# Kernel optimization log

Hardware: AMD Instinct MI355X
Metric: run time of the kernel (lower is better)

The kernel has to match this reference:

```python
import jax, jax.numpy as jnp
import numpy as np

N = 50000      # nodes
E = 600000     # edges
F_IN = 128     # num_features
H = 128        # conv_dim
C = 10         # num_classes


def setup_inputs() -> dict:
    key = jax.random.key(0)
    ks = jax.random.split(key, 16)
    s = 0.05
    return {
        "x": jax.random.normal(ks[0], (N, F_IN), jnp.float32),
        "edge_index": jax.random.randint(ks[1], (2, E), 0, N, dtype=jnp.int32),
        "W1": jax.random.normal(ks[2], (F_IN, H), jnp.float32) * s,
        "b1": jnp.zeros((H,), jnp.float32),
        "W2": jax.random.normal(ks[3], (H, H), jnp.float32) * s,
        "b2": jnp.zeros((H,), jnp.float32),
        "W3": jax.random.normal(ks[4], (H, H), jnp.float32) * s,
        "b3": jnp.zeros((H,), jnp.float32),
        "fw1": jax.random.normal(ks[5], (3 * H, 128), jnp.float32) * s,
        "fb1": jnp.zeros((128,), jnp.float32),
        "fw2": jax.random.normal(ks[6], (128, 64), jnp.float32) * s,
        "fb2": jnp.zeros((64,), jnp.float32),
        "fw3": jax.random.normal(ks[7], (64, C), jnp.float32) * s,
        "fb3": jnp.zeros((C,), jnp.float32),
    }


def reference(x, edge_index, W1, b1, W2, b2, W3, b3, fw1, fb1, fw2, fb2, fw3, fb3):
    n = x.shape[0]
    # GCN normalization with self-loops (improved=False): A_hat = D^-1/2 (A+I) D^-1/2
    loop = jnp.arange(n, dtype=edge_index.dtype)
    src = jnp.concatenate([edge_index[0], loop])   # [E+N]
    tgt = jnp.concatenate([edge_index[1], loop])   # [E+N]
    deg = jax.ops.segment_sum(jnp.ones_like(src, dtype=x.dtype), tgt, num_segments=n)
    dis = jnp.where(deg > 0, jax.lax.rsqrt(jnp.maximum(deg, 1e-12)), 0.0)
    norm = dis[src] * dis[tgt]                     # [E+N]

    def gcn(h, W, b):
        hw = h @ W                                 # [N,H] linear transform first
        msg = norm[:, None] * hw[src]              # gather + edge scale
        return jax.ops.segment_sum(msg, tgt, num_segments=n) + b  # scatter-add

    x1 = jax.nn.relu(gcn(x, W1, b1))
    x2 = jax.nn.relu(gcn(x1, W2, b2))
    x3 = jax.nn.relu(gcn(x2, W3, b3))
    h = jnp.sum(jnp.concatenate([x1, x2, x3], axis=1), axis=0)  # [3H] sum pool
    h = jax.nn.relu(h @ fw1 + fb1)
    h = jax.nn.relu(h @ fw2 + fb2)
    return h @ fw3 + fb3
```

## Files before the change

### kernel.cpp

```cpp
#include <hip/hip_runtime.h>

#define FDIM 128

typedef __attribute__((ext_vector_type(8))) short bf16x8;
typedef __attribute__((ext_vector_type(4))) float f32x4;
typedef __attribute__((ext_vector_type(2))) float f32x2;


__device__ __forceinline__ unsigned int cvt_bf16(float f) {
    unsigned int u = __float_as_uint(f);
    return (u + 0x7fffu + ((u >> 16) & 1u)) >> 16;
}



__global__ void hist_kernel(const int* __restrict__ tgt, int* __restrict__ count, int ne) {
    int e = blockIdx.x * blockDim.x + threadIdx.x;
    if (e < ne) atomicAdd(&count[tgt[e]], 1);
}

__global__ __launch_bounds__(256) void scan1_kernel(const int* __restrict__ count,
                                                    float* __restrict__ dis,
                                                    int* __restrict__ tpre,
                                                    int* __restrict__ bsum, int n) {
    __shared__ int sm[256];
    int tid = threadIdx.x, blk = blockIdx.x;
    int base = blk * 2048 + tid * 8;
    int s = 0;
    #pragma unroll
    for (int q = 0; q < 8; q++) {
        int i = base + q;
        if (i < n) {
            int c = count[i];
            s += c;
            dis[i] = rsqrtf((float)(c + 1));
        }
    }
    sm[tid] = s;
    __syncthreads();
    for (int off = 1; off < 256; off <<= 1) {
        int v = sm[tid];
        int u = (tid >= off) ? sm[tid - off] : 0;
        __syncthreads();
        sm[tid] = v + u;
        __syncthreads();
    }
    tpre[blk * 256 + tid] = (tid == 0) ? 0 : sm[tid - 1];
    if (tid == 255) bsum[blk] = sm[255];
}

__global__ __launch_bounds__(1024) void scan2_kernel(const int* __restrict__ bsum,
                                                     int* __restrict__ bpre,
                                                     int* __restrict__ rowptr,
                                                     float* __restrict__ pool,
                                                     int n, int nb) {
    __shared__ int sm[1024];
    int tid = threadIdx.x;
    if (tid < 384) pool[tid] = 0.f;
    sm[tid] = (tid < nb) ? bsum[tid] : 0;
    __syncthreads();
    for (int off = 1; off < 1024; off <<= 1) {
        int v = sm[tid];
        int u = (tid >= off) ? sm[tid - off] : 0;
        __syncthreads();
        sm[tid] = v + u;
        __syncthreads();
    }
    if (tid < nb) bpre[tid] = (tid == 0) ? 0 : sm[tid - 1];
    if (tid == nb - 1) rowptr[n] = sm[tid];
}

__global__ __launch_bounds__(256) void scan3_kernel(const int* __restrict__ count,
                                                    const int* __restrict__ tpre,
                                                    const int* __restrict__ bpre,
                                                    int* __restrict__ rowptr,
                                                    int* __restrict__ cursor, int n) {
    int tid = threadIdx.x, blk = blockIdx.x;
    int run = bpre[blk] + tpre[blk * 256 + tid];
    int base = blk * 2048 + tid * 8;
    #pragma unroll
    for (int q = 0; q < 8; q++) {
        int i = base + q;
        if (i < n) {
            rowptr[i] = run;
            cursor[i] = run;
            run += count[i];
        }
    }
}

__global__ void fill_kernel(const int* __restrict__ src, const int* __restrict__ tgt,
                            int* __restrict__ cursor, int* __restrict__ csrs, int ne) {
    int e = blockIdx.x * blockDim.x + threadIdx.x;
    if (e < ne) {
        int t = tgt[e];
        int s = src[e];
        int slot = atomicAdd(&cursor[t], 1);
        csrs[slot] = s;
    }
}


__global__ void prep_kernel(const float* __restrict__ W1, const float* __restrict__ W2,
                            const float* __restrict__ W3,
                            unsigned* __restrict__ B1, unsigned* __restrict__ B2,
                            unsigned* __restrict__ B3,
                            unsigned short* __restrict__ g8,
                            int* __restrict__ count, int n) {
    int i = blockIdx.x * blockDim.x + threadIdx.x;
    if (i < 3 * 8192) {
        int w = i >> 13;
        int jj = i & 8191;
        const float* W = (w == 0) ? W1 : (w == 1) ? W2 : W3;
        unsigned* B    = (w == 0) ? B1 : (w == 1) ? B2 : B3;
        int nn = jj >> 6, u = jj & 63;
        float lo = W[(size_t)u * 128 + nn];
        float hi = W[(size_t)(u + 64) * 128 + nn];
        B[jj] = cvt_bf16(lo) | (cvt_bf16(hi) << 16);
    } else if (i < 3 * 8192 + 64) {
        g8[(size_t)n * 64 + (i - 3 * 8192)] = 0;
    } else {
        int k = i - (3 * 8192 + 64);
        if (k < n) count[k] = 0;
    }
}


__global__ __launch_bounds__(256) void gemm_kernel(const unsigned* __restrict__ A16,
                                                   const float* __restrict__ A32,
                                                   const unsigned* __restrict__ Bt16,
                                                   const float* __restrict__ dis,
                                                   unsigned short* __restrict__ g8, int n) {
    int tid  = threadIdx.x;
    int wave = tid >> 6, lane = tid & 63;
    int quad = lane >> 4, r16 = lane & 15;
    int m0 = (blockIdx.x * 4 + wave) * 16;
    if (m0 >= n) return;

    f32x4 acc[8] = {};

    #pragma unroll
    for (int ks = 0; ks < 4; ks++) {
        int m = m0 + r16;
        if (m >= n) m = n - 1;
        int u0 = ks * 16 + quad * 4;
        bf16x8 af;
        if (A32) {
            float4 lo = *(const float4*)(A32 + (size_t)m * 128 + u0);
            float4 hi = *(const float4*)(A32 + (size_t)m * 128 + u0 + 64);
            uint4 p;
            p.x = cvt_bf16(lo.x) | (cvt_bf16(hi.x) << 16);
            p.y = cvt_bf16(lo.y) | (cvt_bf16(hi.y) << 16);
            p.z = cvt_bf16(lo.z) | (cvt_bf16(hi.z) << 16);
            p.w = cvt_bf16(lo.w) | (cvt_bf16(hi.w) << 16);
            af = *(bf16x8*)&p;
        } else {
            uint4 av = *(const uint4*)(A16 + (size_t)m * 64 + u0);
            af = *(bf16x8*)&av;
        }
        #pragma unroll
        for (int t = 0; t < 8; t++) {
            int ncol = t * 16 + r16;
            uint4 bv = *(const uint4*)(Bt16 + (size_t)ncol * 64 + u0);
            bf16x8 bf = *(bf16x8*)&bv;
            acc[t] = __builtin_amdgcn_mfma_f32_16x16x32_bf16(af, bf, acc[t], 0, 0, 0);
        }
    }

    #pragma unroll
    for (int r = 0; r < 4; r++) {
        int row = m0 + quad * 4 + r;
        if (row < n) {
            float dr = dis[row];
            #pragma unroll
            for (int t = 0; t < 4; t++) {
                int p = __builtin_amdgcn_cvt_pk_fp8_f32(dr * acc[t][r], dr * acc[t + 4][r], 0, false);
                g8[(size_t)row * 64 + t * 16 + r16] = (unsigned short)(p & 0xffff);
            }
        }
    }
}


#define AGG_ACC(v)                                                     \
    { f32x2 p;                                                         \
      p = __builtin_amdgcn_cvt_pk_f32_fp8((int)v.x, 0); f0[0]+=p.x; f1[0]+=p.y; \
      p = __builtin_amdgcn_cvt_pk_f32_fp8((int)v.x, 1); f0[1]+=p.x; f1[1]+=p.y; \
      p = __builtin_amdgcn_cvt_pk_f32_fp8((int)v.y, 0); f0[2]+=p.x; f1[2]+=p.y; \
      p = __builtin_amdgcn_cvt_pk_f32_fp8((int)v.y, 1); f0[3]+=p.x; f1[3]+=p.y; \
      p = __builtin_amdgcn_cvt_pk_f32_fp8((int)v.z, 0); f0[4]+=p.x; f1[4]+=p.y; \
      p = __builtin_amdgcn_cvt_pk_f32_fp8((int)v.z, 1); f0[5]+=p.x; f1[5]+=p.y; \
      p = __builtin_amdgcn_cvt_pk_f32_fp8((int)v.w, 0); f0[6]+=p.x; f1[6]+=p.y; \
      p = __builtin_amdgcn_cvt_pk_f32_fp8((int)v.w, 1); f0[7]+=p.x; f1[7]+=p.y; }

#define ISSUE1(buf, ereg, EBASE, mlim)                                 \
    { int e = (EBASE) + j;                                             \
      int s = __shfl(ereg, e);                                         \
      if (e >= (mlim)) s = n;                                          \
      buf = *(const uint4*)(g8 + (size_t)(unsigned)s * 64u + c * 8); }

#define ROUND4(ereg, Q0, mlim)                                         \
    { uint4 u0, u1, u2, u3;                                            \
      ISSUE1(u0, ereg, (Q0) + 0, mlim)                                 \
      if ((mlim) > (Q0) + 8)  ISSUE1(u1, ereg, (Q0) + 8,  mlim)        \
      if ((mlim) > (Q0) + 16) ISSUE1(u2, ereg, (Q0) + 16, mlim)        \
      if ((mlim) > (Q0) + 24) ISSUE1(u3, ereg, (Q0) + 24, mlim)        \
      AGG_ACC(u0)                                                      \
      if ((mlim) > (Q0) + 8)  AGG_ACC(u1)                              \
      if ((mlim) > (Q0) + 16) AGG_ACC(u2)                              \
      if ((mlim) > (Q0) + 24) AGG_ACC(u3) }

__global__ __launch_bounds__(512) void agg_kernel(const unsigned short* __restrict__ g8,
                                                  const float* __restrict__ dis,
                                                  const int* __restrict__ rowptr,
                                                  const int* __restrict__ csrs,
                                                  const float* __restrict__ bias,
                                                  unsigned* __restrict__ out16,
                                                  float* __restrict__ pool,
                                                  int n, int nbase, int nend) {
    __shared__ float lpool[128];
    int tid = threadIdx.x;
    if (tid < 128) lpool[tid] = 0.f;
    __syncthreads();

    int wave = tid >> 6, lane = tid & 63;
    int j = lane >> 3;
    int c = lane & 7;
    int node0 = nbase + (blockIdx.x * 8 + wave) * 4;

    float b0[8], b1[8];
    *(float4*)&b0[0] = *(const float4*)(bias + c * 8);
    *(float4*)&b0[4] = *(const float4*)(bias + c * 8 + 4);
    *(float4*)&b1[0] = *(const float4*)(bias + 64 + c * 8);
    *(float4*)&b1[4] = *(const float4*)(bias + 64 + c * 8 + 4);

    int rpv = 0; float dv = 0.f;
    if (lane <= 4) rpv = rowptr[min(node0 + lane, nend)];
    if (lane < 4)  dv  = dis[min(node0 + lane, n - 1)];

    int er[4];
    #pragma unroll
    for (int i = 0; i < 4; i++) {
        int beg = __shfl(rpv, i);
        er[i] = csrs[beg + lane];
    }

    uint4 c0, c1, c2, c3, sB;
    {
        int deg = __shfl(rpv, 1) - __shfl(rpv, 0);
        int mlim = min(deg, 64);
        int ereg = er[0];
        ISSUE1(c0, ereg, 0, mlim)
        if (deg > 8)  ISSUE1(c1, ereg, 8,  mlim)
        if (deg > 16) ISSUE1(c2, ereg, 16, mlim)
        if (deg > 24) ISSUE1(c3, ereg, 24, mlim)
        int s = (node0 < nend && j == 0) ? node0 : n;
        sB = *(const uint4*)(g8 + (size_t)(unsigned)s * 64u + c * 8);
    }

    float pp0[8] = {}, pp1[8] = {};

    #pragma unroll
    for (int i = 0; i < 4; i++) {
        int node = node0 + i;
        bool ok = node < nend;
        int beg = __shfl(rpv, i);
        int end = __shfl(rpv, i + 1);
        int deg = end - beg;
        float di = __shfl(dv, i);

        float f0[8] = {}, f1[8] = {};
        AGG_ACC(c0)
        if (deg > 8)  AGG_ACC(c1)
        if (deg > 16) AGG_ACC(c2)
        if (deg > 24) AGG_ACC(c3)
        if (deg > 32) {
            int mlim = min(deg, 64);
            ROUND4(er[i], 32, mlim)
            for (int b2 = 64; b2 < deg; b2 += 64) {
                int ereg2 = csrs[beg + b2 + lane];
                int ml2 = min(deg - b2, 64);
                ROUND4(ereg2, 0, ml2)
                if (ml2 > 32) ROUND4(ereg2, 32, ml2)
            }
        }

        uint4 n0v, n1v, n2v, n3v, nS;
        if (i < 3) {
            int nd = __shfl(rpv, i + 2) - end;
            int nml = min(nd, 64);
            int ner = er[i + 1];
            ISSUE1(n0v, ner, 0, nml)
            if (nd > 8)  ISSUE1(n1v, ner, 8,  nml)
            if (nd > 16) ISSUE1(n2v, ner, 16, nml)
            if (nd > 24) ISSUE1(n3v, ner, 24, nml)
            int s = (node + 1 < nend && j == 0) ? (node + 1) : n;
            nS = *(const uint4*)(g8 + (size_t)(unsigned)s * 64u + c * 8);
        }

        #pragma unroll
        for (int k = 0; k < 8; k++) {
            f0[k] += __shfl_xor(f0[k], 8);  f1[k] += __shfl_xor(f1[k], 8);
            f0[k] += __shfl_xor(f0[k], 16); f1[k] += __shfl_xor(f1[k], 16);
            f0[k] += __shfl_xor(f0[k], 32); f1[k] += __shfl_xor(f1[k], 32);
        }
        if (j == 0) AGG_ACC(sB)

        if (ok) {
            float r0[8], r1[8];
            #pragma unroll
            for (int k = 0; k < 8; k++) {
                r0[k] = fmaxf(di * f0[k] + b0[k], 0.f);
                r1[k] = fmaxf(di * f1[k] + b1[k], 0.f);
                pp0[k] += r0[k];
                pp1[k] += r1[k];
            }
            if (out16 && j == 0) {
                uint4 wa, wb;
                wa.x = cvt_bf16(r0[0]) | (cvt_bf16(r1[0]) << 16);
                wa.y = cvt_bf16(r0[1]) | (cvt_bf16(r1[1]) << 16);
                wa.z = cvt_bf16(r0[2]) | (cvt_bf16(r1[2]) << 16);
                wa.w = cvt_bf16(r0[3]) | (cvt_bf16(r1[3]) << 16);
                wb.x = cvt_bf16(r0[4]) | (cvt_bf16(r1[4]) << 16);
                wb.y = cvt_bf16(r0[5]) | (cvt_bf16(r1[5]) << 16);
                wb.z = cvt_bf16(r0[6]) | (cvt_bf16(r1[6]) << 16);
                wb.w = cvt_bf16(r0[7]) | (cvt_bf16(r1[7]) << 16);
                *(uint4*)(out16 + (size_t)node * 64 + c * 8)     = wa;
                *(uint4*)(out16 + (size_t)node * 64 + c * 8 + 4) = wb;
            }
        }

        c0 = n0v; c1 = n1v; c2 = n2v; c3 = n3v; sB = nS;
    }

    if (j == 0) {
        #pragma unroll
        for (int k = 0; k < 8; k++) {
            atomicAdd(&lpool[c * 8 + k],      pp0[k]);
            atomicAdd(&lpool[64 + c * 8 + k], pp1[k]);
        }
    }
    __syncthreads();
    if (tid < 128) atomicAdd(&pool[tid], lpool[tid]);
}


__global__ __launch_bounds__(128) void mlp_kernel(const float* __restrict__ pool,
                                                  const float* __restrict__ fw1, const float* __restrict__ fb1,
                                                  const float* __restrict__ fw2, const float* __restrict__ fb2,
                                                  const float* __restrict__ fw3, const float* __restrict__ fb3,
                                                  float* __restrict__ out) {
    __shared__ float h0[384];
    __shared__ float h1[128];
    __shared__ float h2[64];
    int tid = threadIdx.x;
    for (int i = tid; i < 384; i += 128) h0[i] = pool[i];
    __syncthreads();
    {
        float s = fb1[tid];
        for (int k = 0; k < 384; k++) s += h0[k] * fw1[k * 128 + tid];
        h1[tid] = fmaxf(s, 0.f);
    }
    __syncthreads();
    if (tid < 64) {
        float s = fb2[tid];
        for (int k = 0; k < 128; k++) s += h1[k] * fw2[k * 64 + tid];
        h2[tid] = fmaxf(s, 0.f);
    }
    __syncthreads();
    if (tid < 10) {
        float s = fb3[tid];
        for (int k = 0; k < 64; k++) s += h2[k] * fw3[k * 10 + tid];
        out[tid] = s;
    }
}


extern "C" void kernel_launch(void* const* d_in, const int* in_sizes, int n_in,
                              void* d_out, int out_size, void* d_ws, size_t ws_size,
                              hipStream_t stream) {
    const float* x   = (const float*)d_in[0];
    const int*   ei  = (const int*)d_in[1];
    const float* W1  = (const float*)d_in[2];
    const float* b1  = (const float*)d_in[3];
    const float* W2  = (const float*)d_in[4];
    const float* b2  = (const float*)d_in[5];
    const float* W3  = (const float*)d_in[6];
    const float* b3  = (const float*)d_in[7];
    const float* fw1 = (const float*)d_in[8];
    const float* fb1 = (const float*)d_in[9];
    const float* fw2 = (const float*)d_in[10];
    const float* fb2 = (const float*)d_in[11];
    const float* fw3 = (const float*)d_in[12];
    const float* fb3 = (const float*)d_in[13];
    float* out = (float*)d_out;

    const int n  = in_sizes[0] / FDIM;
    const int ne = in_sizes[1] / 2;
    const int* src = ei;
    const int* tgt = ei + ne;

    char* ws = (char*)d_ws;
    size_t packBytes = (size_t)n * 64 * sizeof(unsigned);
    unsigned* A2   = (unsigned*)ws;  ws += packBytes;
    unsigned* A3   = (unsigned*)ws;  ws += packBytes;
    unsigned short* g8 = (unsigned short*)ws; ws += (((size_t)(n + 1) * 64 * 2 + 127) / 128) * 128;
    unsigned* B1t  = (unsigned*)ws;  ws += 128 * 64 * 4;
    unsigned* B2t  = (unsigned*)ws;  ws += 128 * 64 * 4;
    unsigned* B3t  = (unsigned*)ws;  ws += 128 * 64 * 4;
    float* dis  = (float*)ws;        ws += (size_t)n * 4;
    int* count  = (int*)ws;          ws += (size_t)n * 4;
    int* rowptr = (int*)ws;          ws += ((size_t)(n + 4) * 4 / 16) * 16;
    int* cursor = (int*)ws;          ws += (size_t)n * 4;
    int* csrs   = (int*)ws;          ws += (size_t)(ne + 64) * 4;
    float* pool = (float*)ws;        ws += 384 * 4;
    int nb = (n + 2047) / 2048;
    int* tpre = (int*)ws;            ws += (size_t)nb * 256 * 4;
    int* bsum = (int*)ws;            ws += ((size_t)(nb + 3) / 4) * 16;
    int* bpre = (int*)ws;            ws += ((size_t)(nb + 3) / 4) * 16;

    int prepTotal = 3 * 8192 + 64 + n;
    prep_kernel<<<(prepTotal + 255) / 256, 256, 0, stream>>>(W1, W2, W3, B1t, B2t, B3t, g8, count, n);

    hist_kernel<<<(ne + 255) / 256, 256, 0, stream>>>(tgt, count, ne);
    scan1_kernel<<<nb, 256, 0, stream>>>(count, dis, tpre, bsum, n);
    scan2_kernel<<<1, 1024, 0, stream>>>(bsum, bpre, rowptr, pool, n, nb);
    scan3_kernel<<<nb, 256, 0, stream>>>(count, tpre, bpre, rowptr, cursor, n);
    fill_kernel<<<(ne + 255) / 256, 256, 0, stream>>>(src, tgt, cursor, csrs, ne);

    int gemmGrid = (n + 63) / 64;
    int half = ((n / 2) + 31) & ~31;
    int ag1 = (half + 31) / 32;
    int ag2 = ((n - half) + 31) / 32;

    gemm_kernel<<<gemmGrid, 256, 0, stream>>>((const unsigned*)nullptr, x, B1t, dis, g8, n);
    agg_kernel<<<ag1, 512, 0, stream>>>(g8, dis, rowptr, csrs, b1, A2, pool + 0, n, 0, half);
    agg_kernel<<<ag2, 512, 0, stream>>>(g8, dis, rowptr, csrs, b1, A2, pool + 0, n, half, n);

    gemm_kernel<<<gemmGrid, 256, 0, stream>>>(A2, (const float*)nullptr, B2t, dis, g8, n);
    agg_kernel<<<ag1, 512, 0, stream>>>(g8, dis, rowptr, csrs, b2, A3, pool + 128, n, 0, half);
    agg_kernel<<<ag2, 512, 0, stream>>>(g8, dis, rowptr, csrs, b2, A3, pool + 128, n, half, n);

    gemm_kernel<<<gemmGrid, 256, 0, stream>>>(A3, (const float*)nullptr, B3t, dis, g8, n);
    agg_kernel<<<ag1, 512, 0, stream>>>(g8, dis, rowptr, csrs, b3, (unsigned*)nullptr, pool + 256, n, 0, half);
    agg_kernel<<<ag2, 512, 0, stream>>>(g8, dis, rowptr, csrs, b3, (unsigned*)nullptr, pool + 256, n, half, n);

    mlp_kernel<<<1, 128, 0, stream>>>(pool, fw1, fb1, fw2, fb2, fw3, fb3, out);
}
```

Baseline: 512.2 us.

## Fuse all GCN stages into one cooperative persistent megakernel with grid syncs

Replaces the chain of separate kernels (prep, histogram, three-stage scan, CSR fill, three gemm/aggregate pairs, MLP) with a single cooperative kernel. The stages are separated by grid.sync, and the gemm and aggregation phases become grid-stride loops over tiles. The scan is simplified to one element per thread plus a single-block scan of the per-block sums. The aim is to remove per-launch overhead and inter-kernel gaps. In exchange it pays for twelve grid-wide barriers, runs every phase with one fixed grid and block size, and occupancy may drop from the larger register footprint.

Result: slower. 970.9 us (+89.6%).

```diff
diff --git a/kernel.cpp b/kernel.cpp
--- a/kernel.cpp
+++ b/kernel.cpp
@@ -1,11 +1,13 @@
 #include <hip/hip_runtime.h>
+#include <hip/hip_cooperative_groups.h>
 
 #define FDIM 128
+
+namespace cg = cooperative_groups;
 
 typedef __attribute__((ext_vector_type(8))) short bf16x8;
 typedef __attribute__((ext_vector_type(4))) float f32x4;
 typedef __attribute__((ext_vector_type(2))) float f32x2;
-
 
 __device__ __forceinline__ unsigned int cvt_bf16(float f) {
     unsigned int u = __float_as_uint(f);
@@ -14,168 +16,56 @@
 
 
 
-__global__ void hist_kernel(const int* __restrict__ tgt, int* __restrict__ count, int ne) {
-    int e = blockIdx.x * blockDim.x + threadIdx.x;
-    if (e < ne) atomicAdd(&count[tgt[e]], 1);
-}
-
-__global__ __launch_bounds__(256) void scan1_kernel(const int* __restrict__ count,
-                                                    float* __restrict__ dis,
-                                                    int* __restrict__ tpre,
-                                                    int* __restrict__ bsum, int n) {
-    __shared__ int sm[256];
-    int tid = threadIdx.x, blk = blockIdx.x;
-    int base = blk * 2048 + tid * 8;
-    int s = 0;
-    #pragma unroll
-    for (int q = 0; q < 8; q++) {
-        int i = base + q;
-        if (i < n) {
-            int c = count[i];
-            s += c;
-            dis[i] = rsqrtf((float)(c + 1));
-        }
-    }
-    sm[tid] = s;
-    __syncthreads();
-    for (int off = 1; off < 256; off <<= 1) {
-        int v = sm[tid];
-        int u = (tid >= off) ? sm[tid - off] : 0;
-        __syncthreads();
-        sm[tid] = v + u;
-        __syncthreads();
-    }
-    tpre[blk * 256 + tid] = (tid == 0) ? 0 : sm[tid - 1];
-    if (tid == 255) bsum[blk] = sm[255];
-}
-
-__global__ __launch_bounds__(1024) void scan2_kernel(const int* __restrict__ bsum,
-                                                     int* __restrict__ bpre,
-                                                     int* __restrict__ rowptr,
-                                                     float* __restrict__ pool,
-                                                     int n, int nb) {
-    __shared__ int sm[1024];
+__device__ __forceinline__ void gemm_phase(const unsigned* __restrict__ A16,
+                                           const float* __restrict__ A32,
+                                           const unsigned* __restrict__ Bt16,
+                                           const float* __restrict__ dis,
+                                           unsigned short* __restrict__ g8, int n) {
     int tid = threadIdx.x;
-    if (tid < 384) pool[tid] = 0.f;
-    sm[tid] = (tid < nb) ? bsum[tid] : 0;
-    __syncthreads();
-    for (int off = 1; off < 1024; off <<= 1) {
-        int v = sm[tid];
-        int u = (tid >= off) ? sm[tid - off] : 0;
-        __syncthreads();
-        sm[tid] = v + u;
-        __syncthreads();
-    }
-    if (tid < nb) bpre[tid] = (tid == 0) ? 0 : sm[tid - 1];
-    if (tid == nb - 1) rowptr[n] = sm[tid];
-}
-
-__global__ __launch_bounds__(256) void scan3_kernel(const int* __restrict__ count,
-                                                    const int* __restrict__ tpre,
-                                                    const int* __restrict__ bpre,
-                                                    int* __restrict__ rowptr,
-                                                    int* __restrict__ cursor, int n) {
-    int tid = threadIdx.x, blk = blockIdx.x;
-    int run = bpre[blk] + tpre[blk * 256 + tid];
-    int base = blk * 2048 + tid * 8;
-    #pragma unroll
-    for (int q = 0; q < 8; q++) {
-        int i = base + q;
-        if (i < n) {
-            rowptr[i] = run;
-            cursor[i] = run;
-            run += count[i];
-        }
-    }
-}
-
-__global__ void fill_kernel(const int* __restrict__ src, const int* __restrict__ tgt,
-                            int* __restrict__ cursor, int* __restrict__ csrs, int ne) {
-    int e = blockIdx.x * blockDim.x + threadIdx.x;
-    if (e < ne) {
-        int t = tgt[e];
-        int s = src[e];
-        int slot = atomicAdd(&cursor[t], 1);
-        csrs[slot] = s;
-    }
-}
-
-
-__global__ void prep_kernel(const float* __restrict__ W1, const float* __restrict__ W2,
-                            const float* __restrict__ W3,
-                            unsigned* __restrict__ B1, unsigned* __restrict__ B2,
-                            unsigned* __restrict__ B3,
-                            unsigned short* __restrict__ g8,
-                            int* __restrict__ count, int n) {
-    int i = blockIdx.x * blockDim.x + threadIdx.x;
-    if (i < 3 * 8192) {
-        int w = i >> 13;
-        int jj = i & 8191;
-        const float* W = (w == 0) ? W1 : (w == 1) ? W2 : W3;
-        unsigned* B    = (w == 0) ? B1 : (w == 1) ? B2 : B3;
-        int nn = jj >> 6, u = jj & 63;
-        float lo = W[(size_t)u * 128 + nn];
-        float hi = W[(size_t)(u + 64) * 128 + nn];
-        B[jj] = cvt_bf16(lo) | (cvt_bf16(hi) << 16);
-    } else if (i < 3 * 8192 + 64) {
-        g8[(size_t)n * 64 + (i - 3 * 8192)] = 0;
-    } else {
-        int k = i - (3 * 8192 + 64);
-        if (k < n) count[k] = 0;
-    }
-}
-
-
-__global__ __launch_bounds__(256) void gemm_kernel(const unsigned* __restrict__ A16,
-                                                   const float* __restrict__ A32,
-                                                   const unsigned* __restrict__ Bt16,
-                                                   const float* __restrict__ dis,
-                                                   unsigned short* __restrict__ g8, int n) {
-    int tid  = threadIdx.x;
     int wave = tid >> 6, lane = tid & 63;
     int quad = lane >> 4, r16 = lane & 15;
-    int m0 = (blockIdx.x * 4 + wave) * 16;
-    if (m0 >= n) return;
-
-    f32x4 acc[8] = {};
-
-    #pragma unroll
-    for (int ks = 0; ks < 4; ks++) {
-        int m = m0 + r16;
-        if (m >= n) m = n - 1;
-        int u0 = ks * 16 + quad * 4;
-        bf16x8 af;
-        if (A32) {
-            float4 lo = *(const float4*)(A32 + (size_t)m * 128 + u0);
-            float4 hi = *(const float4*)(A32 + (size_t)m * 128 + u0 + 64);
-            uint4 p;
-            p.x = cvt_bf16(lo.x) | (cvt_bf16(hi.x) << 16);
-            p.y = cvt_bf16(lo.y) | (cvt_bf16(hi.y) << 16);
-            p.z = cvt_bf16(lo.z) | (cvt_bf16(hi.z) << 16);
-            p.w = cvt_bf16(lo.w) | (cvt_bf16(hi.w) << 16);
-            af = *(bf16x8*)&p;
-        } else {
-            uint4 av = *(const uint4*)(A16 + (size_t)m * 64 + u0);
-            af = *(bf16x8*)&av;
-        }
+    int nT = (n + 127) >> 7;
+    for (int T = blockIdx.x; T < nT; T += gridDim.x) {
+        int m0 = T * 128 + wave * 16;
+        if (m0 >= n) continue;
+        f32x4 acc[8] = {};
         #pragma unroll
-        for (int t = 0; t < 8; t++) {
-            int ncol = t * 16 + r16;
-            uint4 bv = *(const uint4*)(Bt16 + (size_t)ncol * 64 + u0);
-            bf16x8 bf = *(bf16x8*)&bv;
-            acc[t] = __builtin_amdgcn_mfma_f32_16x16x32_bf16(af, bf, acc[t], 0, 0, 0);
-        }
-    }
-
-    #pragma unroll
-    for (int r = 0; r < 4; r++) {
-        int row = m0 + quad * 4 + r;
-        if (row < n) {
-            float dr = dis[row];
+        for (int ks = 0; ks < 4; ks++) {
+            int m = m0 + r16;
+            if (m >= n) m = n - 1;
+            int u0 = ks * 16 + quad * 4;
+            bf16x8 af;
+            if (A32) {
+                float4 lo = *(const float4*)(A32 + (size_t)m * 128 + u0);
+                float4 hi = *(const float4*)(A32 + (size_t)m * 128 + u0 + 64);
+                uint4 p;
+                p.x = cvt_bf16(lo.x) | (cvt_bf16(hi.x) << 16);
+                p.y = cvt_bf16(lo.y) | (cvt_bf16(hi.y) << 16);
+                p.z = cvt_bf16(lo.z) | (cvt_bf16(hi.z) << 16);
+                p.w = cvt_bf16(lo.w) | (cvt_bf16(hi.w) << 16);
+                af = *(bf16x8*)&p;
+            } else {
+                uint4 av = *(const uint4*)(A16 + (size_t)m * 64 + u0);
+                af = *(bf16x8*)&av;
+            }
             #pragma unroll
-            for (int t = 0; t < 4; t++) {
-                int p = __builtin_amdgcn_cvt_pk_fp8_f32(dr * acc[t][r], dr * acc[t + 4][r], 0, false);
-                g8[(size_t)row * 64 + t * 16 + r16] = (unsigned short)(p & 0xffff);
+            for (int t = 0; t < 8; t++) {
+                int ncol = t * 16 + r16;
+                uint4 bv = *(const uint4*)(Bt16 + (size_t)ncol * 64 + u0);
+                bf16x8 bf = *(bf16x8*)&bv;
+                acc[t] = __builtin_amdgcn_mfma_f32_16x16x32_bf16(af, bf, acc[t], 0, 0, 0);
+            }
+        }
+        #pragma unroll
+        for (int r = 0; r < 4; r++) {
+            int row = m0 + quad * 4 + r;
+            if (row < n) {
+                float dr = dis[row];
+                #pragma unroll
+                for (int t = 0; t < 4; t++) {
+                    int p = __builtin_amdgcn_cvt_pk_fp8_f32(dr * acc[t][r], dr * acc[t + 4][r], 0, false);
+                    g8[(size_t)row * 64 + t * 16 + r16] = (unsigned short)(p & 0xffff);
+                }
             }
         }
     }
@@ -210,15 +100,14 @@
       if ((mlim) > (Q0) + 16) AGG_ACC(u2)                              \
       if ((mlim) > (Q0) + 24) AGG_ACC(u3) }
 
-__global__ __launch_bounds__(512) void agg_kernel(const unsigned short* __restrict__ g8,
-                                                  const float* __restrict__ dis,
-                                                  const int* __restrict__ rowptr,
-                                                  const int* __restrict__ csrs,
-                                                  const float* __restrict__ bias,
-                                                  unsigned* __restrict__ out16,
-                                                  float* __restrict__ pool,
-                                                  int n, int nbase, int nend) {
-    __shared__ float lpool[128];
+__device__ __forceinline__ void agg_phase(const unsigned short* __restrict__ g8,
+                                          const float* __restrict__ dis,
+                                          const int* __restrict__ rowptr,
+                                          const int* __restrict__ csrs,
+                                          const float* __restrict__ bias,
+                                          unsigned* __restrict__ out16,
+                                          float* __restrict__ poolseg,
+                                          float* lpool, int n) {
     int tid = threadIdx.x;
     if (tid < 128) lpool[tid] = 0.f;
     __syncthreads();
@@ -226,7 +115,6 @@
     int wave = tid >> 6, lane = tid & 63;
     int j = lane >> 3;
     int c = lane & 7;
-    int node0 = nbase + (blockIdx.x * 8 + wave) * 4;
 
     float b0[8], b1[8];
     *(float4*)&b0[0] = *(const float4*)(bias + c * 8);
@@ -234,103 +122,106 @@
     *(float4*)&b1[0] = *(const float4*)(bias + 64 + c * 8);
     *(float4*)&b1[4] = *(const float4*)(bias + 64 + c * 8 + 4);
 
-    int rpv = 0; float dv = 0.f;
-    if (lane <= 4) rpv = rowptr[min(node0 + lane, nend)];
-    if (lane < 4)  dv  = dis[min(node0 + lane, n - 1)];
-
-    int er[4];
-    #pragma unroll
-    for (int i = 0; i < 4; i++) {
-        int beg = __shfl(rpv, i);
-        er[i] = csrs[beg + lane];
-    }
-
-    uint4 c0, c1, c2, c3, sB;
-    {
-        int deg = __shfl(rpv, 1) - __shfl(rpv, 0);
-        int mlim = min(deg, 64);
-        int ereg = er[0];
-        ISSUE1(c0, ereg, 0, mlim)
-        if (deg > 8)  ISSUE1(c1, ereg, 8,  mlim)
-        if (deg > 16) ISSUE1(c2, ereg, 16, mlim)
-        if (deg > 24) ISSUE1(c3, ereg, 24, mlim)
-        int s = (node0 < nend && j == 0) ? node0 : n;
-        sB = *(const uint4*)(g8 + (size_t)(unsigned)s * 64u + c * 8);
-    }
-
     float pp0[8] = {}, pp1[8] = {};
-
-    #pragma unroll
-    for (int i = 0; i < 4; i++) {
-        int node = node0 + i;
-        bool ok = node < nend;
-        int beg = __shfl(rpv, i);
-        int end = __shfl(rpv, i + 1);
-        int deg = end - beg;
-        float di = __shfl(dv, i);
-
-        float f0[8] = {}, f1[8] = {};
-        AGG_ACC(c0)
-        if (deg > 8)  AGG_ACC(c1)
-        if (deg > 16) AGG_ACC(c2)
-        if (deg > 24) AGG_ACC(c3)
-        if (deg > 32) {
+    int nA = (n + 31) >> 5;
+    for (int a = blockIdx.x; a < nA; a += gridDim.x) {
+        int node0 = a * 32 + wave * 4;
+
+        int rpv = 0; float dv = 0.f;
+        if (lane <= 4) rpv = rowptr[min(node0 + lane, n)];
+        if (lane < 4)  dv  = dis[min(node0 + lane, n - 1)];
+
+        int er[4];
+        #pragma unroll
+        for (int i = 0; i < 4; i++) {
+            int beg = __shfl(rpv, i);
+            er[i] = csrs[beg + lane];
+        }
+
+        uint4 c0, c1, c2, c3, sB;
+        {
+            int deg = __shfl(rpv, 1) - __shfl(rpv, 0);
             int mlim = min(deg, 64);
-            ROUND4(er[i], 32, mlim)
-            for (int b2 = 64; b2 < deg; b2 += 64) {
-                int ereg2 = csrs[beg + b2 + lane];
-                int ml2 = min(deg - b2, 64);
-                ROUND4(ereg2, 0, ml2)
-                if (ml2 > 32) ROUND4(ereg2, 32, ml2)
-            }
-        }
-
-        uint4 n0v, n1v, n2v, n3v, nS;
-        if (i < 3) {
-            int nd = __shfl(rpv, i + 2) - end;
-            int nml = min(nd, 64);
-            int ner = er[i + 1];
-            ISSUE1(n0v, ner, 0, nml)
-            if (nd > 8)  ISSUE1(n1v, ner, 8,  nml)
-            if (nd > 16) ISSUE1(n2v, ner, 16, nml)
-            if (nd > 24) ISSUE1(n3v, ner, 24, nml)
-            int s = (node + 1 < nend && j == 0) ? (node + 1) : n;
-            nS = *(const uint4*)(g8 + (size_t)(unsigned)s * 64u + c * 8);
+            int ereg = er[0];
+            ISSUE1(c0, ereg, 0, mlim)
+            if (deg > 8)  ISSUE1(c1, ereg, 8,  mlim)
+            if (deg > 16) ISSUE1(c2, ereg, 16, mlim)
+            if (deg > 24) ISSUE1(c3, ereg, 24, mlim)
+            int s = (node0 < n && j == 0) ? node0 : n;
+            sB = *(const uint4*)(g8 + (size_t)(unsigned)s * 64u + c * 8);
         }
 
         #pragma unroll
-        for (int k = 0; k < 8; k++) {
-            f0[k] += __shfl_xor(f0[k], 8);  f1[k] += __shfl_xor(f1[k], 8);
-            f0[k] += __shfl_xor(f0[k], 16); f1[k] += __shfl_xor(f1[k], 16);
-            f0[k] += __shfl_xor(f0[k], 32); f1[k] += __shfl_xor(f1[k], 32);
-        }
-        if (j == 0) AGG_ACC(sB)
-
-        if (ok) {
-            float r0[8], r1[8];
+        for (int i = 0; i < 4; i++) {
+            int node = node0 + i;
+            bool ok = node < n;
+            int beg = __shfl(rpv, i);
+            int end = __shfl(rpv, i + 1);
+            int deg = end - beg;
+            float di = __shfl(dv, i);
+
+            float f0[8] = {}, f1[8] = {};
+            AGG_ACC(c0)
+            if (deg > 8)  AGG_ACC(c1)
+            if (deg > 16) AGG_ACC(c2)
+            if (deg > 24) AGG_ACC(c3)
+            if (deg > 32) {
+                int mlim = min(deg, 64);
+                ROUND4(er[i], 32, mlim)
+                for (int b2 = 64; b2 < deg; b2 += 64) {
+                    int ereg2 = csrs[beg + b2 + lane];
+                    int ml2 = min(deg - b2, 64);
+                    ROUND4(ereg2, 0, ml2)
+                    if (ml2 > 32) ROUND4(ereg2, 32, ml2)
+                }
+            }
+
+            uint4 n0v, n1v, n2v, n3v, nS;
+            if (i < 3) {
+                int nd = __shfl(rpv, i + 2) - end;
+                int nml = min(nd, 64);
+                int ner = er[i + 1];
+                ISSUE1(n0v, ner, 0, nml)
+                if (nd > 8)  ISSUE1(n1v, ner, 8,  nml)
+                if (nd > 16) ISSUE1(n2v, ner, 16, nml)
+                if (nd > 24) ISSUE1(n3v, ner, 24, nml)
+                int s = (node + 1 < n && j == 0) ? (node + 1) : n;
+                nS = *(const uint4*)(g8 + (size_t)(unsigned)s * 64u + c * 8);
+            }
+
             #pragma unroll
             for (int k = 0; k < 8; k++) {
-                r0[k] = fmaxf(di * f0[k] + b0[k], 0.f);
-                r1[k] = fmaxf(di * f1[k] + b1[k], 0.f);
-                pp0[k] += r0[k];
-                pp1[k] += r1[k];
-            }
-            if (out16 && j == 0) {
-                uint4 wa, wb;
-                wa.x = cvt_bf16(r0[0]) | (cvt_bf16(r1[0]) << 16);
-                wa.y = cvt_bf16(r0[1]) | (cvt_bf16(r1[1]) << 16);
-                wa.z = cvt_bf16(r0[2]) | (cvt_bf16(r1[2]) << 16);
-                wa.w = cvt_bf16(r0[3]) | (cvt_bf16(r1[3]) << 16);
-                wb.x = cvt_bf16(r0[4]) | (cvt_bf16(r1[4]) << 16);
-                wb.y = cvt_bf16(r0[5]) | (cvt_bf16(r1[5]) << 16);
-                wb.z = cvt_bf16(r0[6]) | (cvt_bf16(r1[6]) << 16);
-                wb.w = cvt_bf16(r0[7]) | (cvt_bf16(r1[7]) << 16);
-                *(uint4*)(out16 + (size_t)node * 64 + c * 8)     = wa;
-                *(uint4*)(out16 + (size_t)node * 64 + c * 8 + 4) = wb;
-            }
-        }
-
-        c0 = n0v; c1 = n1v; c2 = n2v; c3 = n3v; sB = nS;
+                f0[k] += __shfl_xor(f0[k], 8);  f1[k] += __shfl_xor(f1[k], 8);
+                f0[k] += __shfl_xor(f0[k], 16); f1[k] += __shfl_xor(f1[k], 16);
+                f0[k] += __shfl_xor(f0[k], 32); f1[k] += __shfl_xor(f1[k], 32);
+            }
+            if (j == 0) AGG_ACC(sB)
+
+            if (ok) {
+                float r0[8], r1[8];
+                #pragma unroll
+                for (int k = 0; k < 8; k++) {
+                    r0[k] = fmaxf(di * f0[k] + b0[k], 0.f);
+                    r1[k] = fmaxf(di * f1[k] + b1[k], 0.f);
+                    pp0[k] += r0[k];
+                    pp1[k] += r1[k];
+                }
+                if (out16 && j == 0) {
+                    uint4 wa, wb;
+                    wa.x = cvt_bf16(r0[0]) | (cvt_bf16(r1[0]) << 16);
+                    wa.y = cvt_bf16(r0[1]) | (cvt_bf16(r1[1]) << 16);
+                    wa.z = cvt_bf16(r0[2]) | (cvt_bf16(r1[2]) << 16);
+                    wa.w = cvt_bf16(r0[3]) | (cvt_bf16(r1[3]) << 16);
+                    wb.x = cvt_bf16(r0[4]) | (cvt_bf16(r1[4]) << 16);
+                    wb.y = cvt_bf16(r0[5]) | (cvt_bf16(r1[5]) << 16);
+                    wb.z = cvt_bf16(r0[6]) | (cvt_bf16(r1[6]) << 16);
+                    wb.w = cvt_bf16(r0[7]) | (cvt_bf16(r1[7]) << 16);
+                    *(uint4*)(out16 + (size_t)node * 64 + c * 8)     = wa;
+                    *(uint4*)(out16 + (size_t)node * 64 + c * 8 + 4) = wb;
+                }
+            }
+            c0 = n0v; c1 = n1v; c2 = n2v; c3 = n3v; sB = nS;
+        }
     }
 
     if (j == 0) {
@@ -341,37 +232,146 @@
         }
     }
     __syncthreads();
-    if (tid < 128) atomicAdd(&pool[tid], lpool[tid]);
+    if (tid < 128) atomicAdd(&poolseg[tid], lpool[tid]);
 }
 
 
-__global__ __launch_bounds__(128) void mlp_kernel(const float* __restrict__ pool,
-                                                  const float* __restrict__ fw1, const float* __restrict__ fb1,
-                                                  const float* __restrict__ fw2, const float* __restrict__ fb2,
-                                                  const float* __restrict__ fw3, const float* __restrict__ fb3,
-                                                  float* __restrict__ out) {
+__global__ __launch_bounds__(512, 4) void mega_kernel(
+    const float* __restrict__ x, const int* __restrict__ src, const int* __restrict__ tgt,
+    const float* __restrict__ W1, const float* __restrict__ b1,
+    const float* __restrict__ W2, const float* __restrict__ b2,
+    const float* __restrict__ W3, const float* __restrict__ b3,
+    const float* __restrict__ fw1, const float* __restrict__ fb1,
+    const float* __restrict__ fw2, const float* __restrict__ fb2,
+    const float* __restrict__ fw3, const float* __restrict__ fb3,
+    float* __restrict__ out,
+    unsigned* __restrict__ B1t, unsigned* __restrict__ B2t, unsigned* __restrict__ B3t,
+    unsigned short* __restrict__ g8, unsigned* __restrict__ A2, unsigned* __restrict__ A3,
+    float* __restrict__ dis, int* __restrict__ count, int* __restrict__ rowptr,
+    int* __restrict__ cursor, int* __restrict__ csrs, float* __restrict__ pool,
+    int* __restrict__ bsum, int* __restrict__ bpre,
+    int n, int ne)
+{
+    cg::grid_group grid = cg::this_grid();
+    const int tid = threadIdx.x;
+    const int bid = blockIdx.x;
+    const int G   = gridDim.x;
+    const int gstride = G * 512;
+
+    __shared__ int   sm[512];
+    __shared__ float lpool[128];
     __shared__ float h0[384];
     __shared__ float h1[128];
     __shared__ float h2[64];
-    int tid = threadIdx.x;
-    for (int i = tid; i < 384; i += 128) h0[i] = pool[i];
+
+    {
+        int total0 = 24640 + n + 384;
+        for (int i = bid * 512 + tid; i < total0; i += gstride) {
+            if (i < 24576) {
+                int w = i >> 13, jj = i & 8191;
+                const float* W = (w == 0) ? W1 : (w == 1) ? W2 : W3;
+                unsigned* B    = (w == 0) ? B1t : (w == 1) ? B2t : B3t;
+                int nn = jj >> 6, u = jj & 63;
+                float lo = W[(size_t)u * 128 + nn];
+                float hi = W[(size_t)(u + 64) * 128 + nn];
+                B[jj] = cvt_bf16(lo) | (cvt_bf16(hi) << 16);
+            } else if (i < 24640) {
+                g8[(size_t)n * 64 + (i - 24576)] = 0;
+            } else if (i < 24640 + n) {
+                count[i - 24640] = 0;
+            } else {
+                pool[i - 24640 - n] = 0.f;
+            }
+        }
+    }
+    grid.sync();
+
+    for (int e = bid * 512 + tid; e < ne; e += gstride)
+        atomicAdd(&count[tgt[e]], 1);
+    grid.sync();
+
+    int i_elem = bid * 512 + tid;
+    int cval = (i_elem < n) ? count[i_elem] : 0;
+    if (i_elem < n) dis[i_elem] = rsqrtf((float)(cval + 1));
+    sm[tid] = cval;
     __syncthreads();
-    {
-        float s = fb1[tid];
-        for (int k = 0; k < 384; k++) s += h0[k] * fw1[k * 128 + tid];
-        h1[tid] = fmaxf(s, 0.f);
-    }
-    __syncthreads();
-    if (tid < 64) {
-        float s = fb2[tid];
-        for (int k = 0; k < 128; k++) s += h1[k] * fw2[k * 64 + tid];
-        h2[tid] = fmaxf(s, 0.f);
-    }
-    __syncthreads();
-    if (tid < 10) {
-        float s = fb3[tid];
-        for (int k = 0; k < 64; k++) s += h2[k] * fw3[k * 10 + tid];
-        out[tid] = s;
+    for (int off = 1; off < 512; off <<= 1) {
+        int v = sm[tid];
+        int u = (tid >= off) ? sm[tid - off] : 0;
+        __syncthreads();
+        sm[tid] = v + u;
+        __syncthreads();
+    }
+    int epre = sm[tid] - cval;
+    if (tid == 511) bsum[bid] = sm[511];
+    grid.sync();
+
+    if (bid == 0) {
+        int v = (tid < G) ? bsum[tid] : 0;
+        sm[tid] = v;
+        __syncthreads();
+        for (int off = 1; off < 512; off <<= 1) {
+            int a = sm[tid];
+            int u = (tid >= off) ? sm[tid - off] : 0;
+            __syncthreads();
+            sm[tid] = a + u;
+            __syncthreads();
+        }
+        bpre[tid] = sm[tid] - v;
+        if (tid == 511) rowptr[n] = sm[511];
+    }
+    grid.sync();
+
+    if (i_elem < n) {
+        int run = bpre[bid] + epre;
+        rowptr[i_elem] = run;
+        cursor[i_elem] = run;
+    }
+    grid.sync();
+
+    for (int e = bid * 512 + tid; e < ne; e += gstride) {
+        int t = tgt[e];
+        int s = src[e];
+        int slot = atomicAdd(&cursor[t], 1);
+        csrs[slot] = s;
+    }
+    grid.sync();
+
+    gemm_phase(nullptr, x, B1t, dis, g8, n);
+    grid.sync();
+    agg_phase(g8, dis, rowptr, csrs, b1, A2, pool + 0, lpool, n);
+    grid.sync();
+
+    gemm_phase(A2, nullptr, B2t, dis, g8, n);
+    grid.sync();
+    agg_phase(g8, dis, rowptr, csrs, b2, A3, pool + 128, lpool, n);
+    grid.sync();
+
+    gemm_phase(A3, nullptr, B3t, dis, g8, n);
+    grid.sync();
+    agg_phase(g8, dis, rowptr, csrs, b3, (unsigned*)nullptr, pool + 256, lpool, n);
+    grid.sync();
+
+    if (bid == 0) {
+        if (tid < 384) h0[tid] = pool[tid];
+        __syncthreads();
+        if (tid < 128) {
+            float s = fb1[tid];
+            for (int k = 0; k < 384; k++) s += h0[k] * fw1[k * 128 + tid];
+            h1[tid] = fmaxf(s, 0.f);
+        }
+        __syncthreads();
+        if (tid < 64) {
+            float s = fb2[tid];
+            for (int k = 0; k < 128; k++) s += h1[k] * fw2[k * 64 + tid];
+            h2[tid] = fmaxf(s, 0.f);
+        }
+        __syncthreads();
+        if (tid < 10) {
+            float s = fb3[tid];
+            for (int k = 0; k < 64; k++) s += h2[k] * fw3[k * 10 + tid];
+            out[tid] = s;
+        }
     }
 }
 
@@ -395,8 +395,8 @@
     const float* fb3 = (const float*)d_in[13];
     float* out = (float*)d_out;
 
-    const int n  = in_sizes[0] / FDIM;
-    const int ne = in_sizes[1] / 2;
+    int n  = in_sizes[0] / FDIM;
+    int ne = in_sizes[1] / 2;
     const int* src = ei;
     const int* tgt = ei + ne;
 
@@ -414,36 +414,25 @@
     int* cursor = (int*)ws;          ws += (size_t)n * 4;
     int* csrs   = (int*)ws;          ws += (size_t)(ne + 64) * 4;
     float* pool = (float*)ws;        ws += 384 * 4;
-    int nb = (n + 2047) / 2048;
-    int* tpre = (int*)ws;            ws += (size_t)nb * 256 * 4;
-    int* bsum = (int*)ws;            ws += ((size_t)(nb + 3) / 4) * 16;
-    int* bpre = (int*)ws;            ws += ((size_t)(nb + 3) / 4) * 16;
-
-    int prepTotal = 3 * 8192 + 64 + n;
-    prep_kernel<<<(prepTotal + 255) / 256, 256, 0, stream>>>(W1, W2, W3, B1t, B2t, B3t, g8, count, n);
-
-    hist_kernel<<<(ne + 255) / 256, 256, 0, stream>>>(tgt, count, ne);
-    scan1_kernel<<<nb, 256, 0, stream>>>(count, dis, tpre, bsum, n);
-    scan2_kernel<<<1, 1024, 0, stream>>>(bsum, bpre, rowptr, pool, n, nb);
-    scan3_kernel<<<nb, 256, 0, stream>>>(count, tpre, bpre, rowptr, cursor, n);
-    fill_kernel<<<(ne + 255) / 256, 256, 0, stream>>>(src, tgt, cursor, csrs, ne);
-
-    int gemmGrid = (n + 63) / 64;
-    int half = ((n / 2) + 31) & ~31;
-    int ag1 = (half + 31) / 32;
-    int ag2 = ((n - half) + 31) / 32;
-
-    gemm_kernel<<<gemmGrid, 256, 0, stream>>>((const unsigned*)nullptr, x, B1t, dis, g8, n);
-    agg_kernel<<<ag1, 512, 0, stream>>>(g8, dis, rowptr, csrs, b1, A2, pool + 0, n, 0, half);
-    agg_kernel<<<ag2, 512, 0, stream>>>(g8, dis, rowptr, csrs, b1, A2, pool + 0, n, half, n);
-
-    gemm_kernel<<<gemmGrid, 256, 0, stream>>>(A2, (const float*)nullptr, B2t, dis, g8, n);
-    agg_kernel<<<ag1, 512, 0, stream>>>(g8, dis, rowptr, csrs, b2, A3, pool + 128, n, 0, half);
-    agg_kernel<<<ag2, 512, 0, stream>>>(g8, dis, rowptr, csrs, b2, A3, pool + 128, n, half, n);
-
-    gemm_kernel<<<gemmGrid, 256, 0, stream>>>(A3, (const float*)nullptr, B3t, dis, g8, n);
-    agg_kernel<<<ag1, 512, 0, stream>>>(g8, dis, rowptr, csrs, b3, (unsigned*)nullptr, pool + 256, n, 0, half);
-    agg_kernel<<<ag2, 512, 0, stream>>>(g8, dis, rowptr, csrs, b3, (unsigned*)nullptr, pool + 256, n, half, n);
-
-    mlp_kernel<<<1, 128, 0, stream>>>(pool, fw1, fb1, fw2, fb2, fw3, fb3, out);
+    int* bsum   = (int*)ws;          ws += 512 * 4;
+    int* bpre   = (int*)ws;          ws += 512 * 4;
+
+    int maxPerCU = 0;
+    hipError_t oe = hipOccupancyMaxActiveBlocksPerMultiprocessor(&maxPerCU, mega_kernel, 512, 0);
+    int G = (oe == hipSuccess && maxPerCU > 0) ? maxPerCU * 256 : 256;
+    if (G > 512) G = 512;
+    if (G < 256) G = 256;
+
+    void* kargs[] = {
+        (void*)&x, (void*)&src, (void*)&tgt,
+        (void*)&W1, (void*)&b1, (void*)&W2, (void*)&b2, (void*)&W3, (void*)&b3,
+        (void*)&fw1, (void*)&fb1, (void*)&fw2, (void*)&fb2, (void*)&fw3, (void*)&fb3,
+        (void*)&out,
+        (void*)&B1t, (void*)&B2t, (void*)&B3t,
+        (void*)&g8, (void*)&A2, (void*)&A3,
+        (void*)&dis, (void*)&count, (void*)&rowptr, (void*)&cursor, (void*)&csrs,
+        (void*)&pool, (void*)&bsum, (void*)&bpre,
+        (void*)&n, (void*)&ne
+    };
+    hipLaunchCooperativeKernel(mega_kernel, dim3(G), dim3(512), kargs, 0, stream);
 }
```
